# Performance work log

Measured on AMD Instinct MI355X. Metric: run time of the kernel, lower is better.

## Reference

```python
import jax, jax.numpy as jnp
import numpy as np

N_NODES = 1048576
N_GRAPHS = 4096
NODES_PER_GRAPH = N_NODES // N_GRAPHS
N_EDGES = 8388608
F_IN = 16
HID = 32


def _glorot(k, shp):
    return jax.random.normal(k, shp, jnp.float32) * np.float32(np.sqrt(2.0 / (shp[-2] + shp[-1])))


def setup_inputs() -> dict:
    key = jax.random.key(0)
    ks = jax.random.split(key, 8)
    d = F_IN + HID  # DCRNN gate convs act on cat([X, H])
    return {
        "x": jax.random.normal(ks[0], (N_NODES, F_IN), jnp.float32),
        "edge_index": jax.random.randint(ks[1], (2, N_EDGES), 0, N_NODES),
        "edge_weight": jax.random.uniform(ks[2], (N_EDGES,), jnp.float32),
        "batch": jnp.repeat(jnp.arange(N_GRAPHS), NODES_PER_GRAPH),
        "W_z": _glorot(ks[3], (2, 1, d, HID)),
        "b_z": jnp.zeros((HID,), jnp.float32),
        "W_r": _glorot(ks[4], (2, 1, d, HID)),
        "b_r": jnp.zeros((HID,), jnp.float32),
        "W_h": _glorot(ks[5], (2, 1, d, HID)),
        "b_h": jnp.zeros((HID,), jnp.float32),
        "W_lin": _glorot(ks[6], (HID, 1)),
        "b_lin": jnp.zeros((1,), jnp.float32),
    }


def _dconv_k1(X, W, b):
    # torch_geometric_temporal DConv with K=1: the diffusion loop never runs,
    # so H = X @ W[0,0] + X @ W[1,0] + b (edge_index/edge_weight unused).
    return X @ (W[0, 0] + W[1, 0]) + b


def reference(x, edge_index, edge_weight, batch, W_z, b_z, W_r, b_r, W_h, b_h, W_lin, b_lin):
    del edge_index, edge_weight  # mathematically unused when K=1
    h0 = jnp.zeros((x.shape[0], HID), x.dtype)  # DCRNN hidden state default
    xh = jnp.concatenate([x, h0], axis=1)
    Z = jax.nn.sigmoid(_dconv_k1(xh, W_z, b_z))
    R = jax.nn.sigmoid(_dconv_k1(xh, W_r, b_r))
    xhr = jnp.concatenate([x, h0 * R], axis=1)
    H_tilde = jnp.tanh(_dconv_k1(xhr, W_h, b_h))
    H = Z * h0 + (1.0 - Z) * H_tilde  # (N, 32)
    h = jax.nn.relu(H)
    h = h @ W_lin + b_lin  # (N, 1)
    # global_mean_pool over per-node graph ids
    sums = jax.ops.segment_sum(h, batch, num_segments=N_GRAPHS)
    cnts = jax.ops.segment_sum(jnp.ones((h.shape[0], 1), h.dtype), batch, num_segments=N_GRAPHS)
    return sums / jnp.maximum(cnts, 1.0)  # (N_GRAPHS, 1)
```

## Files before the change

### kernel.cpp

```cpp
#include <hip/hip_runtime.h>

#define N_GRAPHS  4096
#define NPG       256
#define F_IN      16
#define HID       32
#define LOG2E     1.4426950408889634f

#define WS_FLOATS 1121

typedef _Float16 half8   __attribute__((ext_vector_type(8)));
typedef float    float4v __attribute__((ext_vector_type(4)));

#if __has_builtin(__builtin_amdgcn_exp2f)
#define EXP2(x) __builtin_amdgcn_exp2f(x)
#else
#define EXP2(x) exp2f(x)
#endif

union FragU { uint4 u; half8 h; };

__device__ __forceinline__ uint4 make_frag(int f, int l,
    const float* __restrict__ Wz, const float* __restrict__ Wh)
{
    const int q = l >> 4, m = l & 15;
    const int c = (f & 1) * 16 + m;
    const float s = (f < 2) ? LOG2E : 2.0f * LOG2E;
    const float* W = (f < 2) ? Wz : Wh;
    FragU u;
#pragma unroll
    for (int j = 0; j < 8; ++j) {
        const int k = (q & 1) * 8 + j;
        u.h[j] = (_Float16)((W[k * 32 + c] + W[1536 + k * 32 + c]) * s);
    }
    return u.u;
}

__global__ __launch_bounds__(256) void prep_kernel(
    const float* __restrict__ Wz, const float* __restrict__ bz,
    const float* __restrict__ Wh, const float* __restrict__ bh,
    const float* __restrict__ Wlin, const float* __restrict__ blin,
    float* __restrict__ w)
{
    const int t = threadIdx.x;
    ((uint4*)w)[t] = make_frag(t >> 6, t & 63, Wz, Wh);
    if (t < HID) {
        w[1024 + t] = bz[t] * LOG2E;
        w[1056 + t] = bh[t] * (2.0f * LOG2E);
        w[1088 + t] = Wlin[t];
    }
    if (t == 0) w[1120] = blin[0];
}

__device__ __forceinline__ float gate_term(float az, float ah, float wl, float osum)
{
    const float e1 = EXP2(az);
    const float e2 = EXP2(fminf(ah, 126.0f));
    const float r  = __builtin_amdgcn_rcpf((1.0f + e1) * (e2 + 1.0f));
    float v = (e2 - 1.0f) * r;
    v = v > 0.0f ? v : 0.0f;
    return fmaf(v, wl, osum);
}

__device__ __forceinline__ void gcn_body(const float* __restrict__ x,
                                         const float* __restrict__ w,
                                         float* __restrict__ out, int g, int t)
{
    const int lane = t & 63, wv = t >> 6;
    const int q = lane >> 4, m = lane & 15;

    const uint4* bq = (const uint4*)w;
    FragU u0, u1, u2, u3;
    u0.u = bq[lane];       u1.u = bq[64 + lane];
    u2.u = bq[128 + lane]; u3.u = bq[192 + lane];
    const half8 Bz0 = u0.h, Bz1 = u1.h, Bh0 = u2.h, Bh1 = u3.h;

    const float bz0 = w[1024 + m], bz1 = w[1040 + m];
    const float bh0 = w[1056 + m], bh1 = w[1072 + m];
    const float wl0 = w[1088 + m], wl1 = w[1104 + m];

    const float* xw = x + ((size_t)g * NPG + wv * 64 + m) * F_IN + (q & 1) * 8;
    float4 c0 = *(const float4*)(xw);
    float4 c1 = *(const float4*)(xw + 4);
    const bool lo_lane = (q >= 2);
    float osum = 0.0f;

#pragma unroll
    for (int it = 0; it < 4; ++it) {
        float4 n0 = c0, n1 = c1;
        if (it < 3) {
            n0 = *(const float4*)(xw + (it + 1) * 256);
            n1 = *(const float4*)(xw + (it + 1) * 256 + 4);
        }
        const float xf[8] = { c0.x, c0.y, c0.z, c0.w, c1.x, c1.y, c1.z, c1.w };
        half8 A;
#pragma unroll
        for (int j = 0; j < 8; ++j) {
            _Float16 h = (_Float16)xf[j];
            if (lo_lane) h = (_Float16)(xf[j] - (float)h);
            A[j] = h;
        }

        float4v az0 = { bz0, bz0, bz0, bz0 };
        float4v az1 = { bz1, bz1, bz1, bz1 };
        float4v ah0 = { bh0, bh0, bh0, bh0 };
        float4v ah1 = { bh1, bh1, bh1, bh1 };
        az0 = __builtin_amdgcn_mfma_f32_16x16x32_f16(A, Bz0, az0, 0, 0, 0);
        ah0 = __builtin_amdgcn_mfma_f32_16x16x32_f16(A, Bh0, ah0, 0, 0, 0);
        az1 = __builtin_amdgcn_mfma_f32_16x16x32_f16(A, Bz1, az1, 0, 0, 0);
        ah1 = __builtin_amdgcn_mfma_f32_16x16x32_f16(A, Bh1, ah1, 0, 0, 0);

#pragma unroll
        for (int i = 0; i < 4; ++i) {
            osum = gate_term(az0[i], ah0[i], wl0, osum);
            osum = gate_term(az1[i], ah1[i], wl1, osum);
        }
        c0 = n0; c1 = n1;
    }

#pragma unroll
    for (int off = 32; off > 0; off >>= 1)
        osum += __shfl_down(osum, off, 64);
    __shared__ float part[4];
    if (lane == 0) part[wv] = osum;
    __syncthreads();
    if (t == 0)
        out[g] = (part[0] + part[1] + part[2] + part[3]) * (1.0f / (float)NPG)
               + w[1120];
}

__global__ __launch_bounds__(256, 6) void gcn_main(
    const float* __restrict__ x, const float* __restrict__ w, float* __restrict__ out)
{
    gcn_body(x, w, out, blockIdx.x, threadIdx.x);
}

__global__ __launch_bounds__(256, 6) void gcn_main_lds(
    const float* __restrict__ x,
    const float* __restrict__ Wz, const float* __restrict__ bz,
    const float* __restrict__ Wh, const float* __restrict__ bh,
    const float* __restrict__ Wlin, const float* __restrict__ blin,
    float* __restrict__ out)
{
    __shared__ __attribute__((aligned(16))) float w[WS_FLOATS];
    const int t = threadIdx.x;
    ((uint4*)w)[t] = make_frag(t >> 6, t & 63, Wz, Wh);
    if (t < HID) {
        w[1024 + t] = bz[t] * LOG2E;
        w[1056 + t] = bh[t] * (2.0f * LOG2E);
        w[1088 + t] = Wlin[t];
    }
    if (t == 0) w[1120] = blin[0];
    __syncthreads();
    gcn_body(x, w, out, blockIdx.x, t);
}

extern "C" void kernel_launch(void* const* d_in, const int* in_sizes, int n_in,
                              void* d_out, int out_size, void* d_ws, size_t ws_size,
                              hipStream_t stream)
{
    const float* x    = (const float*)d_in[0];
    const float* Wz   = (const float*)d_in[4];
    const float* bz   = (const float*)d_in[5];
    const float* Wh   = (const float*)d_in[8];
    const float* bh   = (const float*)d_in[9];
    const float* Wlin = (const float*)d_in[10];
    const float* blin = (const float*)d_in[11];
    float* out = (float*)d_out;

    if (ws_size >= WS_FLOATS * sizeof(float)) {
        float* w = (float*)d_ws;
        prep_kernel<<<1, 256, 0, stream>>>(Wz, bz, Wh, bh, Wlin, blin, w);
        gcn_main<<<N_GRAPHS, NPG, 0, stream>>>(x, w, out);
    } else {
        gcn_main_lds<<<N_GRAPHS, NPG, 0, stream>>>(x, Wz, bz, Wh, bh, Wlin, blin, out);
    }
}
```

Before: 166.1 us.

## Fuse weight prep into main kernel and pack fp16 splits with cvt_pkrtz

Drops the separate prep kernel and workspace path. Each thread now builds its own fp16 MFMA weight fragments straight from global weights, and the biases are loaded per block. The hi/lo fp16 split of x now uses packed round-toward-zero conversions and a branchless select. This removes one kernel launch and its dependency, at the cost of redundant weight loads and conversions in every block. Rounding toward zero for the hi part changes numerics slightly, but the lo residual compensates.

```diff
diff --git a/kernel.cpp b/kernel.cpp
--- a/kernel.cpp
+++ b/kernel.cpp
@@ -6,9 +6,8 @@
 #define HID       32
 #define LOG2E     1.4426950408889634f
 
-#define WS_FLOATS 1121
-
 typedef _Float16 half8   __attribute__((ext_vector_type(8)));
+typedef __fp16   fp16x2  __attribute__((ext_vector_type(2)));
 typedef float    float4v __attribute__((ext_vector_type(4)));
 
 #if __has_builtin(__builtin_amdgcn_exp2f)
@@ -17,38 +16,21 @@
 #define EXP2(x) exp2f(x)
 #endif
 
-union FragU { uint4 u; half8 h; };
+union AU { uint4 u; half8 h; };
 
-__device__ __forceinline__ uint4 make_frag(int f, int l,
-    const float* __restrict__ Wz, const float* __restrict__ Wh)
-{
-    const int q = l >> 4, m = l & 15;
-    const int c = (f & 1) * 16 + m;
-    const float s = (f < 2) ? LOG2E : 2.0f * LOG2E;
-    const float* W = (f < 2) ? Wz : Wh;
-    FragU u;
+__device__ __forceinline__ half8 pack8(const float f[8]) {
+    half8 r;
+#if __has_builtin(__builtin_amdgcn_cvt_pkrtz)
+    fp16x2 p;
+    p = __builtin_amdgcn_cvt_pkrtz(f[0], f[1]); r[0] = (_Float16)p.x; r[1] = (_Float16)p.y;
+    p = __builtin_amdgcn_cvt_pkrtz(f[2], f[3]); r[2] = (_Float16)p.x; r[3] = (_Float16)p.y;
+    p = __builtin_amdgcn_cvt_pkrtz(f[4], f[5]); r[4] = (_Float16)p.x; r[5] = (_Float16)p.y;
+    p = __builtin_amdgcn_cvt_pkrtz(f[6], f[7]); r[6] = (_Float16)p.x; r[7] = (_Float16)p.y;
+#else
 #pragma unroll
-    for (int j = 0; j < 8; ++j) {
-        const int k = (q & 1) * 8 + j;
-        u.h[j] = (_Float16)((W[k * 32 + c] + W[1536 + k * 32 + c]) * s);
-    }
-    return u.u;
-}
-
-__global__ __launch_bounds__(256) void prep_kernel(
-    const float* __restrict__ Wz, const float* __restrict__ bz,
-    const float* __restrict__ Wh, const float* __restrict__ bh,
-    const float* __restrict__ Wlin, const float* __restrict__ blin,
-    float* __restrict__ w)
-{
-    const int t = threadIdx.x;
-    ((uint4*)w)[t] = make_frag(t >> 6, t & 63, Wz, Wh);
-    if (t < HID) {
-        w[1024 + t] = bz[t] * LOG2E;
-        w[1056 + t] = bh[t] * (2.0f * LOG2E);
-        w[1088 + t] = Wlin[t];
-    }
-    if (t == 0) w[1120] = blin[0];
+    for (int j = 0; j < 8; ++j) r[j] = (_Float16)f[j];
+#endif
+    return r;
 }
 
 __device__ __forceinline__ float gate_term(float az, float ah, float wl, float osum)
@@ -61,22 +43,33 @@
     return fmaf(v, wl, osum);
 }
 
-__device__ __forceinline__ void gcn_body(const float* __restrict__ x,
-                                         const float* __restrict__ w,
-                                         float* __restrict__ out, int g, int t)
+__global__ __launch_bounds__(256, 6) void gcn_fused(
+    const float* __restrict__ x,
+    const float* __restrict__ Wz, const float* __restrict__ bz,
+    const float* __restrict__ Wh, const float* __restrict__ bh,
+    const float* __restrict__ Wlin, const float* __restrict__ blin,
+    float* __restrict__ out)
 {
+    const int t = threadIdx.x, g = blockIdx.x;
     const int lane = t & 63, wv = t >> 6;
     const int q = lane >> 4, m = lane & 15;
 
-    const uint4* bq = (const uint4*)w;
-    FragU u0, u1, u2, u3;
-    u0.u = bq[lane];       u1.u = bq[64 + lane];
-    u2.u = bq[128 + lane]; u3.u = bq[192 + lane];
-    const half8 Bz0 = u0.h, Bz1 = u1.h, Bh0 = u2.h, Bh1 = u3.h;
-
-    const float bz0 = w[1024 + m], bz1 = w[1040 + m];
-    const float bh0 = w[1056 + m], bh1 = w[1072 + m];
-    const float wl0 = w[1088 + m], wl1 = w[1104 + m];
+    half8 Bz0, Bz1, Bh0, Bh1;
+    {
+        const int krow = (q & 1) * 8;
+#pragma unroll
+        for (int j = 0; j < 8; ++j) {
+            const float* wzp = Wz + (krow + j) * 32;
+            const float* whp = Wh + (krow + j) * 32;
+            Bz0[j] = (_Float16)((wzp[m]      + wzp[1536 + m])      * LOG2E);
+            Bz1[j] = (_Float16)((wzp[16 + m] + wzp[1536 + 16 + m]) * LOG2E);
+            Bh0[j] = (_Float16)((whp[m]      + whp[1536 + m])      * (2.0f * LOG2E));
+            Bh1[j] = (_Float16)((whp[16 + m] + whp[1536 + 16 + m]) * (2.0f * LOG2E));
+        }
+    }
+    const float bz0 = bz[m] * LOG2E,          bz1 = bz[16 + m] * LOG2E;
+    const float bh0 = bh[m] * (2.0f * LOG2E), bh1 = bh[16 + m] * (2.0f * LOG2E);
+    const float wl0 = Wlin[m],                wl1 = Wlin[16 + m];
 
     const float* xw = x + ((size_t)g * NPG + wv * 64 + m) * F_IN + (q & 1) * 8;
     float4 c0 = *(const float4*)(xw);
@@ -92,13 +85,18 @@
             n1 = *(const float4*)(xw + (it + 1) * 256 + 4);
         }
         const float xf[8] = { c0.x, c0.y, c0.z, c0.w, c1.x, c1.y, c1.z, c1.w };
-        half8 A;
+
+        AU hi, lo, a;
+        hi.h = pack8(xf);
+        float rf[8];
 #pragma unroll
-        for (int j = 0; j < 8; ++j) {
-            _Float16 h = (_Float16)xf[j];
-            if (lo_lane) h = (_Float16)(xf[j] - (float)h);
-            A[j] = h;
-        }
+        for (int j = 0; j < 8; ++j) rf[j] = xf[j] - (float)hi.h[j];
+        lo.h = pack8(rf);
+        a.u.x = lo_lane ? lo.u.x : hi.u.x;
+        a.u.y = lo_lane ? lo.u.y : hi.u.y;
+        a.u.z = lo_lane ? lo.u.z : hi.u.z;
+        a.u.w = lo_lane ? lo.u.w : hi.u.w;
+        const half8 A = a.h;
 
         float4v az0 = { bz0, bz0, bz0, bz0 };
         float4v az1 = { bz1, bz1, bz1, bz1 };
@@ -125,33 +123,7 @@
     __syncthreads();
     if (t == 0)
         out[g] = (part[0] + part[1] + part[2] + part[3]) * (1.0f / (float)NPG)
-               + w[1120];
-}
-
-__global__ __launch_bounds__(256, 6) void gcn_main(
-    const float* __restrict__ x, const float* __restrict__ w, float* __restrict__ out)
-{
-    gcn_body(x, w, out, blockIdx.x, threadIdx.x);
-}
-
-__global__ __launch_bounds__(256, 6) void gcn_main_lds(
-    const float* __restrict__ x,
-    const float* __restrict__ Wz, const float* __restrict__ bz,
-    const float* __restrict__ Wh, const float* __restrict__ bh,
-    const float* __restrict__ Wlin, const float* __restrict__ blin,
-    float* __restrict__ out)
-{
-    __shared__ __attribute__((aligned(16))) float w[WS_FLOATS];
-    const int t = threadIdx.x;
-    ((uint4*)w)[t] = make_frag(t >> 6, t & 63, Wz, Wh);
-    if (t < HID) {
-        w[1024 + t] = bz[t] * LOG2E;
-        w[1056 + t] = bh[t] * (2.0f * LOG2E);
-        w[1088 + t] = Wlin[t];
-    }
-    if (t == 0) w[1120] = blin[0];
-    __syncthreads();
-    gcn_body(x, w, out, blockIdx.x, t);
+               + blin[0];
 }
 
 extern "C" void kernel_launch(void* const* d_in, const int* in_sizes, int n_in,
@@ -167,11 +139,5 @@
     const float* blin = (const float*)d_in[11];
     float* out = (float*)d_out;
 
-    if (ws_size >= WS_FLOATS * sizeof(float)) {
-        float* w = (float*)d_ws;
-        prep_kernel<<<1, 256, 0, stream>>>(Wz, bz, Wh, bh, Wlin, blin, w);
-        gcn_main<<<N_GRAPHS, NPG, 0, stream>>>(x, w, out);
-    } else {
-        gcn_main_lds<<<N_GRAPHS, NPG, 0, stream>>>(x, Wz, bz, Wh, bh, Wlin, blin, out);
-    }
+    gcn_fused<<<N_GRAPHS, NPG, 0, stream>>>(x, Wz, bz, Wh, bh, Wlin, blin, out);
 }
```

Result: slower. 180.7 us (+8.8%).
